# Kernel tuning notes

Hardware: AMD Instinct MI355X
Metric: run time of the kernel (lower is better)

## Reference

```python
import jax, jax.numpy as jnp
import numpy as np

E = 8          # num_experts
K = 2          # num_experts_per_tok
H = 768        # hidden_size
F = 3072       # ffn_hidden_size
B, S = 2, 1024


def setup_inputs() -> dict:
    key = jax.random.key(0)
    ks = jax.random.split(key, 5)
    scale_r = 1.0 / np.sqrt(H)
    scale_1 = 1.0 / np.sqrt(H)
    scale_2 = 1.0 / np.sqrt(F)
    return {
        "hidden_states": jax.random.normal(ks[0], (B, S, H), dtype=jnp.float32),
        "router_w": jax.random.normal(ks[1], (E, H), dtype=jnp.float32) * scale_r,
        "w1": jax.random.normal(ks[2], (E, F, H), dtype=jnp.float32) * scale_1,
        "b1": jnp.zeros((E, F), dtype=jnp.float32),
        "w2": jax.random.normal(ks[3], (E, H, F), dtype=jnp.float32) * scale_2,
        "b2": jnp.zeros((E, H), dtype=jnp.float32),
    }


def reference(hidden_states, router_w, w1, b1, w2, b2):
    b, s, h = hidden_states.shape
    x = hidden_states.reshape(-1, h)                      # [T, H]

    # Router: logits -> top-k -> softmax over the selected k logits
    logits = jnp.einsum('th,eh->te', x, router_w)          # [T, E]
    top_vals, top_idx = jax.lax.top_k(logits, K)           # [T, K]
    probs = jax.nn.softmax(top_vals, axis=-1)              # [T, K]

    # Combine weights per (token, expert): sum of top-k probs routed to e
    one_hot = jax.nn.one_hot(top_idx, E, dtype=probs.dtype)  # [T, K, E]
    combine = jnp.einsum('tk,tke->te', probs, one_hot)       # [T, E]

    # Dense per-expert FFN (GEMM -> exact GELU -> GEMM), combined by weights
    hmid = jnp.einsum('th,efh->tef', x, w1) + b1[None]       # [T, E, F]
    hmid = jax.nn.gelu(hmid, approximate=False)
    y = jnp.einsum('tef,ehf->teh', hmid, w2) + b2[None]      # [T, E, H]
    out = jnp.einsum('teh,te->th', y, combine)               # [T, H]

    return out.reshape(b, s, h)
```

## Files before the change

### kernel.cpp

```cpp
#include <hip/hip_runtime.h>
#include <hip/hip_bf16.h>
#include <math.h>

#define T_TOK 2048
#define EXP   8
#define HID   768
#define FFN   3072
#define MAXTILES 40

typedef __bf16 bf16x8 __attribute__((ext_vector_type(8)));
typedef float  f32x4  __attribute__((ext_vector_type(4)));
typedef short  s16x8  __attribute__((ext_vector_type(8)));

#define WS_CNT      0
#define WS_OFFS     64
#define WS_NTILES   128
#define WS_TILEE    256
#define WS_TILEROW  1280
#define WS_TKE      4096
#define WS_TKP      20480
#define WS_TOKIDS   36864
#define WS_PW       53248
#define WS_XPK      131072
#define WS_W1PK     (WS_XPK  + 15728640)
#define WS_W2PK     (WS_W1PK + 75497472)
#define WS_HMA      (WS_W2PK + 75497472)

__device__ __forceinline__ void gload16(const void* g, void* l) {
    __builtin_amdgcn_global_load_lds((__attribute__((address_space(1))) void*)g,
                                     (__attribute__((address_space(3))) void*)l,
                                     16, 0, 0);
}

__device__ __forceinline__ void split_bf16(float f, short& hi, short& lo) {
    unsigned u  = __float_as_uint(f);
    unsigned h  = (u + 0x8000u) >> 16;
    float    hf = __uint_as_float(h << 16);
    float    lf = f - hf;
    unsigned l  = (__float_as_uint(lf) + 0x8000u) >> 16;
    hi = (short)h; lo = (short)l;
}

__device__ __forceinline__ float gelu_exact(float v) {
    return 0.5f * v * (1.0f + erff(v * 0.70710678118654752f));
}

__global__ void k_init(float* __restrict__ out, int* __restrict__ cnt) {
    int idx = blockIdx.x * blockDim.x + threadIdx.x;
    const int n = T_TOK * HID;
    for (int i = idx; i < n; i += gridDim.x * blockDim.x) out[i] = 0.f;
    if (idx < EXP) cnt[idx] = 0;
}

__global__ __launch_bounds__(256) void k_router(
    const float* __restrict__ x, const float* __restrict__ rw,
    int* __restrict__ tk_e, float* __restrict__ tk_p, int* __restrict__ cnt)
{
    int wave = threadIdx.x >> 6;
    int lane = threadIdx.x & 63;
    int t = blockIdx.x * 4 + wave;
    if (t >= T_TOK) return;

    float acc[EXP];
#pragma unroll
    for (int e = 0; e < EXP; ++e) acc[e] = 0.f;
    const float* xr = x + (size_t)t * HID;
#pragma unroll
    for (int i = 0; i < HID / 64; ++i) {
        int k = i * 64 + lane;
        float xv = xr[k];
#pragma unroll
        for (int e = 0; e < EXP; ++e) acc[e] += xv * rw[e * HID + k];
    }
#pragma unroll
    for (int e = 0; e < EXP; ++e) {
        float v = acc[e];
#pragma unroll
        for (int off = 32; off > 0; off >>= 1) v += __shfl_xor(v, off);
        acc[e] = v;
    }
    int e0 = 0; float v0 = acc[0];
#pragma unroll
    for (int e = 1; e < EXP; ++e) if (acc[e] > v0) { v0 = acc[e]; e0 = e; }
    int e1 = -1; float v1 = -INFINITY;
#pragma unroll
    for (int e = 0; e < EXP; ++e) if (e != e0 && acc[e] > v1) { v1 = acc[e]; e1 = e; }
    float ex = expf(v1 - v0);
    float p0 = 1.f / (1.f + ex);
    float p1 = ex / (1.f + ex);

    if (lane == 0) {
        tk_e[t * 2 + 0] = e0; tk_e[t * 2 + 1] = e1;
        tk_p[t * 2 + 0] = p0; tk_p[t * 2 + 1] = p1;
        atomicAdd(&cnt[e0], 1);
        atomicAdd(&cnt[e1], 1);
    }
}

__global__ __launch_bounds__(256) void k_scatter(
    const int* __restrict__ cnt, int* __restrict__ offs, int* __restrict__ nTiles,
    int* __restrict__ tileE, int* __restrict__ tileRow,
    const int* __restrict__ tk_e, const float* __restrict__ tk_p,
    int* __restrict__ token_ids, float* __restrict__ pw)
{
    __shared__ int fill[EXP];
    __shared__ int offsS[EXP + 1];
    if (threadIdx.x == 0) {
        int o = 0;
        for (int e = 0; e < EXP; ++e) { offsS[e] = o; offs[e] = o; o += cnt[e]; }
        offsS[EXP] = o; offs[EXP] = o;
        int nt = 0;
        for (int e = 0; e < EXP; ++e)
            for (int r = 0; r < cnt[e]; r += 128) {
                tileE[nt] = e; tileRow[nt] = offsS[e] + r; ++nt;
            }
        *nTiles = nt;
    }
    if (threadIdx.x < EXP) fill[threadIdx.x] = 0;
    __syncthreads();
    for (int t = threadIdx.x; t < T_TOK; t += 256) {
#pragma unroll
        for (int kk = 0; kk < 2; ++kk) {
            int e = tk_e[t * 2 + kk];
            int slot = atomicAdd(&fill[e], 1);
            int g = offsS[e] + slot;
            token_ids[g] = t;
            pw[g] = tk_p[t * 2 + kk];
        }
    }
}

__global__ __launch_bounds__(256) void k_packw(
    const float* __restrict__ W, short* __restrict__ pk, int N, int K)
{
    int unit = blockIdx.x * 4 + (threadIdx.x >> 6);
    int lane = threadIdx.x & 63;
    int NTN = N >> 7, NTK = K >> 5;
    int half = unit & 1;
    int u2   = unit >> 1;
    int kt   = u2 % NTK;
    int ent  = u2 / NTK;
    int nt   = ent % NTN;
    int e    = ent / NTN;
    int row  = nt * 128 + half * 64 + lane;

    const float* src = W + ((size_t)e * N + row) * K + kt * 32;
    s16x8 h4[4], l4v[4];
#pragma unroll
    for (int c = 0; c < 32; c += 4) {
        float4 f = *(const float4*)(src + c);
        short hh, ll;
        split_bf16(f.x, hh, ll); h4[c >> 3][(c & 7) + 0] = hh; l4v[c >> 3][(c & 7) + 0] = ll;
        split_bf16(f.y, hh, ll); h4[c >> 3][(c & 7) + 1] = hh; l4v[c >> 3][(c & 7) + 1] = ll;
        split_bf16(f.z, hh, ll); h4[c >> 3][(c & 7) + 2] = hh; l4v[c >> 3][(c & 7) + 2] = ll;
        split_bf16(f.w, hh, ll); h4[c >> 3][(c & 7) + 3] = hh; l4v[c >> 3][(c & 7) + 3] = ll;
    }
    short* base = pk + ((size_t)ent * NTK + kt) * 8192;
#pragma unroll
    for (int kg = 0; kg < 4; ++kg) {
        *(s16x8*)(base + (0 * 8 + kg * 2 + half) * 512 + lane * 8) = h4[kg];
        *(s16x8*)(base + (1 * 8 + kg * 2 + half) * 512 + lane * 8) = l4v[kg];
    }
}

__global__ __launch_bounds__(256) void k_packx(
    const float* __restrict__ x, const int* __restrict__ token_ids,
    const int* __restrict__ tileE, const int* __restrict__ tileRow,
    const int* __restrict__ offs, const int* __restrict__ nTiles,
    short* __restrict__ xpk)
{
    int unit = blockIdx.x * 4 + (threadIdx.x >> 6);
    int lane = threadIdx.x & 63;
    int half = unit & 1;
    int u2   = unit >> 1;
    int kt   = u2 % 24;
    int tile = u2 / 24;
    if (tile >= *nTiles) return;
    int e = tileE[tile];
    int rowEnd = offs[e + 1];
    int g = min(tileRow[tile] + half * 64 + lane, rowEnd - 1);
    int t = token_ids[g];

    const float* src = x + (size_t)t * HID + kt * 32;
    s16x8 h4[4], l4v[4];
#pragma unroll
    for (int c = 0; c < 32; c += 4) {
        float4 f = *(const float4*)(src + c);
        short hh, ll;
        split_bf16(f.x, hh, ll); h4[c >> 3][(c & 7) + 0] = hh; l4v[c >> 3][(c & 7) + 0] = ll;
        split_bf16(f.y, hh, ll); h4[c >> 3][(c & 7) + 1] = hh; l4v[c >> 3][(c & 7) + 1] = ll;
        split_bf16(f.z, hh, ll); h4[c >> 3][(c & 7) + 2] = hh; l4v[c >> 3][(c & 7) + 2] = ll;
        split_bf16(f.w, hh, ll); h4[c >> 3][(c & 7) + 3] = hh; l4v[c >> 3][(c & 7) + 3] = ll;
    }
    short* base = xpk + ((size_t)tile * 24 + kt) * 8192;
#pragma unroll
    for (int kg = 0; kg < 4; ++kg) {
        *(s16x8*)(base + (0 * 8 + kg * 2 + half) * 512 + lane * 8) = h4[kg];
        *(s16x8*)(base + (1 * 8 + kg * 2 + half) * 512 + lane * 8) = l4v[kg];
    }
}


#define DBUF 16384

__global__ __launch_bounds__(256, 2) void k_gemm1_mfma(
    const short* __restrict__ xpk, const short* __restrict__ w1pk,
    const float* __restrict__ b1, short* __restrict__ hmA,
    const int* __restrict__ tileE, const int* __restrict__ tileRow,
    const int* __restrict__ offs, const int* __restrict__ nTiles)
{
    const int lin = blockIdx.x;
    const int swz = (lin & 7) * 120 + (lin >> 3);
    const int bx   = swz % 24;
    const int tile = swz / 24;
    if (tile >= *nTiles) return;
    const int e = tileE[tile];
    const int rowBase = tileRow[tile];
    const int rowEnd = offs[e + 1];
    const int n0 = bx * 128;

    __shared__ __align__(16) short S[2][DBUF];

    const int tid = threadIdx.x;
    const int lane = tid & 63;
    const int w = tid >> 6;
    const int wm = w & 1, wn = w >> 1;
    const int l15 = lane & 15, l4 = lane >> 4;

    const short* jsrc[8];
    int jdst[8];
#pragma unroll
    for (int j = 0; j < 8; ++j) {
        int s = w + j * 4;
        int ab = s >> 4, p = (s >> 3) & 1, kg = (s >> 1) & 3, h = s & 1;
        jdst[j] = ((ab * 2 + p) * 4 + kg) * 1024 + h * 512;
        if (ab == 0)
            jsrc[j] = xpk + (size_t)tile * 24 * 8192 + s * 512 + lane * 8;
        else
            jsrc[j] = w1pk + ((size_t)(e * 24 + bx) * 24) * 8192
                      + (s - 16) * 512 + lane * 8;
    }

    f32x4 acc[4][4] = {};

#pragma unroll
    for (int j = 0; j < 8; ++j) gload16(jsrc[j], (void*)&S[0][jdst[j]]);
    __syncthreads();

    const int NT = 24;
    for (int kt = 0; kt < NT; ++kt) {
        int cur = kt & 1;
        if (kt + 1 < NT) {
            size_t k0 = (size_t)(kt + 1) * 8192;
#pragma unroll
            for (int j = 0; j < 8; ++j) gload16(jsrc[j] + k0, (void*)&S[cur ^ 1][jdst[j]]);
        }
        const short* base = S[cur];
        bf16x8 ah[4], al[4], bh[4], bl[4];
#pragma unroll
        for (int mf = 0; mf < 4; ++mf) {
            int r = wm * 64 + mf * 16 + l15;
            ah[mf] = *(const bf16x8*)(base + (0 * 4 + l4) * 1024 + r * 8);
            al[mf] = *(const bf16x8*)(base + (1 * 4 + l4) * 1024 + r * 8);
        }
#pragma unroll
        for (int nf = 0; nf < 4; ++nf) {
            int c = wn * 64 + nf * 16 + l15;
            bh[nf] = *(const bf16x8*)(base + (2 * 4 + l4) * 1024 + c * 8);
            bl[nf] = *(const bf16x8*)(base + (3 * 4 + l4) * 1024 + c * 8);
        }
#pragma unroll
        for (int mf = 0; mf < 4; ++mf)
#pragma unroll
            for (int nf = 0; nf < 4; ++nf)
                acc[mf][nf] = __builtin_amdgcn_mfma_f32_16x16x32_bf16(ah[mf], bh[nf], acc[mf][nf], 0, 0, 0);
#pragma unroll
        for (int mf = 0; mf < 4; ++mf)
#pragma unroll
            for (int nf = 0; nf < 4; ++nf)
                acc[mf][nf] = __builtin_amdgcn_mfma_f32_16x16x32_bf16(ah[mf], bl[nf], acc[mf][nf], 0, 0, 0);
#pragma unroll
        for (int mf = 0; mf < 4; ++mf)
#pragma unroll
            for (int nf = 0; nf < 4; ++nf)
                acc[mf][nf] = __builtin_amdgcn_mfma_f32_16x16x32_bf16(al[mf], bh[nf], acc[mf][nf], 0, 0, 0);
        __syncthreads();
    }

#pragma unroll
    for (int mf = 0; mf < 4; ++mf)
#pragma unroll
        for (int nf = 0; nf < 4; ++nf) {
            int f = n0 + wn * 64 + nf * 16 + l15;
            float bias = b1[e * FFN + f];
            int ktf = f >> 5, kg = (f >> 3) & 3, sh = f & 7;
            size_t kbase = ((size_t)tile * 96 + ktf) * 8192 + (kg * 2) * 512 + sh;
#pragma unroll
            for (int j = 0; j < 4; ++j) {
                int row = wm * 64 + mf * 16 + l4 * 4 + j;
                if (rowBase + row < rowEnd) {
                    float v = gelu_exact(acc[mf][nf][j] + bias);
                    short hi, lo;
                    split_bf16(v, hi, lo);
                    size_t o = kbase + (row >> 6) * 512 + (row & 63) * 8;
                    hmA[o] = hi;
                    hmA[o + 4096] = lo;
                }
            }
        }
}

__global__ __launch_bounds__(256, 2) void k_gemm2_mfma(
    const short* __restrict__ hmA, const short* __restrict__ w2pk,
    const float* __restrict__ b2, float* __restrict__ out,
    const int* __restrict__ token_ids, const float* __restrict__ pw,
    const int* __restrict__ tileE, const int* __restrict__ tileRow,
    const int* __restrict__ offs, const int* __restrict__ nTiles)
{
    const int lin = blockIdx.x;
    const int swz = (lin & 7) * 120 + (lin >> 3);
    const int sub = swz % 24;
    const int bx  = sub % 6;
    const int z   = sub / 6;
    const int tile = swz / 24;
    if (tile >= *nTiles) return;
    const int e = tileE[tile];
    const int rowBase = tileRow[tile];
    const int rowEnd = offs[e + 1];
    const int n0 = bx * 128;

    __shared__ __align__(16) short S[2][DBUF];

    const int tid = threadIdx.x;
    const int lane = tid & 63;
    const int w = tid >> 6;
    const int wm = w & 1, wn = w >> 1;
    const int l15 = lane & 15, l4 = lane >> 4;

    const short* jsrc[8];
    int jdst[8];
#pragma unroll
    for (int j = 0; j < 8; ++j) {
        int s = w + j * 4;
        int ab = s >> 4, p = (s >> 3) & 1, kg = (s >> 1) & 3, h = s & 1;
        jdst[j] = ((ab * 2 + p) * 4 + kg) * 1024 + h * 512;
        if (ab == 0)
            jsrc[j] = hmA + ((size_t)tile * 96 + z * 24) * 8192 + s * 512 + lane * 8;
        else
            jsrc[j] = w2pk + ((size_t)(e * 6 + bx) * 96 + z * 24) * 8192
                      + (s - 16) * 512 + lane * 8;
    }

    f32x4 acc[4][4] = {};

#pragma unroll
    for (int j = 0; j < 8; ++j) gload16(jsrc[j], (void*)&S[0][jdst[j]]);
    __syncthreads();

    const int NT = 24;
    for (int kt = 0; kt < NT; ++kt) {
        int cur = kt & 1;
        if (kt + 1 < NT) {
            size_t k0 = (size_t)(kt + 1) * 8192;
#pragma unroll
            for (int j = 0; j < 8; ++j) gload16(jsrc[j] + k0, (void*)&S[cur ^ 1][jdst[j]]);
        }
        const short* base = S[cur];
        bf16x8 ah[4], al[4], bh[4], bl[4];
#pragma unroll
        for (int mf = 0; mf < 4; ++mf) {
            int r = wm * 64 + mf * 16 + l15;
            ah[mf] = *(const bf16x8*)(base + (0 * 4 + l4) * 1024 + r * 8);
            al[mf] = *(const bf16x8*)(base + (1 * 4 + l4) * 1024 + r * 8);
        }
#pragma unroll
        for (int nf = 0; nf < 4; ++nf) {
            int c = wn * 64 + nf * 16 + l15;
            bh[nf] = *(const bf16x8*)(base + (2 * 4 + l4) * 1024 + c * 8);
            bl[nf] = *(const bf16x8*)(base + (3 * 4 + l4) * 1024 + c * 8);
        }
#pragma unroll
        for (int mf = 0; mf < 4; ++mf)
#pragma unroll
            for (int nf = 0; nf < 4; ++nf)
                acc[mf][nf] = __builtin_amdgcn_mfma_f32_16x16x32_bf16(ah[mf], bh[nf], acc[mf][nf], 0, 0, 0);
#pragma unroll
        for (int mf = 0; mf < 4; ++mf)
#pragma unroll
            for (int nf = 0; nf < 4; ++nf)
                acc[mf][nf] = __builtin_amdgcn_mfma_f32_16x16x32_bf16(ah[mf], bl[nf], acc[mf][nf], 0, 0, 0);
#pragma unroll
        for (int mf = 0; mf < 4; ++mf)
#pragma unroll
            for (int nf = 0; nf < 4; ++nf)
                acc[mf][nf] = __builtin_amdgcn_mfma_f32_16x16x32_bf16(al[mf], bh[nf], acc[mf][nf], 0, 0, 0);
        __syncthreads();
    }

#pragma unroll
    for (int mf = 0; mf < 4; ++mf)
#pragma unroll
        for (int nf = 0; nf < 4; ++nf) {
            int h = n0 + wn * 64 + nf * 16 + l15;
            float bias = (z == 0) ? b2[e * HID + h] : 0.f;
#pragma unroll
            for (int j = 0; j < 4; ++j) {
                int g = rowBase + wm * 64 + mf * 16 + l4 * 4 + j;
                if (g < rowEnd) {
                    int t = token_ids[g];
                    float p = pw[g];
                    atomicAdd(&out[(size_t)t * HID + h], (acc[mf][nf][j] + bias) * p);
                }
            }
        }
}

extern "C" void kernel_launch(void* const* d_in, const int* in_sizes, int n_in,
                              void* d_out, int out_size, void* d_ws, size_t ws_size,
                              hipStream_t stream) {
    const float* x  = (const float*)d_in[0];
    const float* rw = (const float*)d_in[1];
    const float* w1 = (const float*)d_in[2];
    const float* b1 = (const float*)d_in[3];
    const float* w2 = (const float*)d_in[4];
    const float* b2 = (const float*)d_in[5];
    float* out = (float*)d_out;

    char* ws = (char*)d_ws;
    int*   cnt       = (int*)(ws + WS_CNT);
    int*   offs      = (int*)(ws + WS_OFFS);
    int*   nTiles    = (int*)(ws + WS_NTILES);
    int*   tileE     = (int*)(ws + WS_TILEE);
    int*   tileRow   = (int*)(ws + WS_TILEROW);
    int*   tk_e      = (int*)(ws + WS_TKE);
    float* tk_p      = (float*)(ws + WS_TKP);
    int*   token_ids = (int*)(ws + WS_TOKIDS);
    float* pw        = (float*)(ws + WS_PW);
    short* xpk  = (short*)(ws + WS_XPK);
    short* w1pk = (short*)(ws + WS_W1PK);
    short* w2pk = (short*)(ws + WS_W2PK);
    short* hmA  = (short*)(ws + WS_HMA);

    k_init<<<1024, 256, 0, stream>>>(out, cnt);
    k_router<<<T_TOK / 4, 256, 0, stream>>>(x, rw, tk_e, tk_p, cnt);
    k_scatter<<<1, 256, 0, stream>>>(cnt, offs, nTiles, tileE, tileRow,
                                     tk_e, tk_p, token_ids, pw);
    k_packw<<<2304, 256, 0, stream>>>(w1, w1pk, FFN, HID);
    k_packw<<<2304, 256, 0, stream>>>(w2, w2pk, HID, FFN);
    k_packx<<<480, 256, 0, stream>>>(x, token_ids, tileE, tileRow, offs, nTiles, xpk);
    k_gemm1_mfma<<<960, 256, 0, stream>>>(
        xpk, w1pk, b1, hmA, tileE, tileRow, offs, nTiles);
    k_gemm2_mfma<<<960, 256, 0, stream>>>(
        hmA, w2pk, b2, out, token_ids, pw, tileE, tileRow, offs, nTiles);
}
```

Measured before the change: 503.1 us.

## Triple-buffer LDS in both expert GEMMs with vmcnt-based waits

Both grouped MFMA GEMM kernels move from double to triple LDS buffering and prefetch two K-steps ahead. The per-iteration __syncthreads is replaced by an explicit s_waitcnt vmcnt plus a single s_barrier, so one tile's loads can stay in flight while the current tile is computed. This is meant to hide global-to-LDS latency and cut barrier stalls. LDS use per block goes from 64KB to 96KB and the min-blocks hint is dropped, which may reduce occupancy, and correctness depends on the hand-counted vmcnt matching the direct-to-LDS loads.

```diff
diff --git a/kernel.cpp b/kernel.cpp
--- a/kernel.cpp
+++ b/kernel.cpp
@@ -203,7 +203,7 @@
 
 #define DBUF 16384
 
-__global__ __launch_bounds__(256, 2) void k_gemm1_mfma(
+__global__ __launch_bounds__(256) void k_gemm1_mfma(
     const short* __restrict__ xpk, const short* __restrict__ w1pk,
     const float* __restrict__ b1, short* __restrict__ hmA,
     const int* __restrict__ tileE, const int* __restrict__ tileRow,
@@ -219,7 +219,7 @@
     const int rowEnd = offs[e + 1];
     const int n0 = bx * 128;
 
-    __shared__ __align__(16) short S[2][DBUF];
+    __shared__ __align__(16) short S[3][DBUF];
 
     const int tid = threadIdx.x;
     const int lane = tid & 63;
@@ -243,17 +243,22 @@
 
     f32x4 acc[4][4] = {};
 
+    const int NT = 24;
 #pragma unroll
     for (int j = 0; j < 8; ++j) gload16(jsrc[j], (void*)&S[0][jdst[j]]);
-    __syncthreads();
-
-    const int NT = 24;
+#pragma unroll
+    for (int j = 0; j < 8; ++j) gload16(jsrc[j] + 8192, (void*)&S[1][jdst[j]]);
+
+    int cur = 0;
     for (int kt = 0; kt < NT; ++kt) {
-        int cur = kt & 1;
-        if (kt + 1 < NT) {
-            size_t k0 = (size_t)(kt + 1) * 8192;
-#pragma unroll
-            for (int j = 0; j < 8; ++j) gload16(jsrc[j] + k0, (void*)&S[cur ^ 1][jdst[j]]);
+        if (kt + 1 < NT) asm volatile("s_waitcnt vmcnt(8)" ::: "memory");
+        else             asm volatile("s_waitcnt vmcnt(0)" ::: "memory");
+        __builtin_amdgcn_s_barrier();
+        if (kt + 2 < NT) {
+            int nb = cur + 2; if (nb >= 3) nb -= 3;
+            size_t k0 = (size_t)(kt + 2) * 8192;
+#pragma unroll
+            for (int j = 0; j < 8; ++j) gload16(jsrc[j] + k0, (void*)&S[nb][jdst[j]]);
         }
         const short* base = S[cur];
         bf16x8 ah[4], al[4], bh[4], bl[4];
@@ -284,7 +289,7 @@
 #pragma unroll
             for (int nf = 0; nf < 4; ++nf)
                 acc[mf][nf] = __builtin_amdgcn_mfma_f32_16x16x32_bf16(al[mf], bh[nf], acc[mf][nf], 0, 0, 0);
-        __syncthreads();
+        ++cur; if (cur >= 3) cur -= 3;
     }
 
 #pragma unroll
@@ -310,7 +315,7 @@
         }
 }
 
-__global__ __launch_bounds__(256, 2) void k_gemm2_mfma(
+__global__ __launch_bounds__(256) void k_gemm2_mfma(
     const short* __restrict__ hmA, const short* __restrict__ w2pk,
     const float* __restrict__ b2, float* __restrict__ out,
     const int* __restrict__ token_ids, const float* __restrict__ pw,
@@ -329,7 +334,7 @@
     const int rowEnd = offs[e + 1];
     const int n0 = bx * 128;
 
-    __shared__ __align__(16) short S[2][DBUF];
+    __shared__ __align__(16) short S[3][DBUF];
 
     const int tid = threadIdx.x;
     const int lane = tid & 63;
@@ -353,17 +358,22 @@
 
     f32x4 acc[4][4] = {};
 
+    const int NT = 24;
 #pragma unroll
     for (int j = 0; j < 8; ++j) gload16(jsrc[j], (void*)&S[0][jdst[j]]);
-    __syncthreads();
-
-    const int NT = 24;
+#pragma unroll
+    for (int j = 0; j < 8; ++j) gload16(jsrc[j] + 8192, (void*)&S[1][jdst[j]]);
+
+    int cur = 0;
     for (int kt = 0; kt < NT; ++kt) {
-        int cur = kt & 1;
-        if (kt + 1 < NT) {
-            size_t k0 = (size_t)(kt + 1) * 8192;
-#pragma unroll
-            for (int j = 0; j < 8; ++j) gload16(jsrc[j] + k0, (void*)&S[cur ^ 1][jdst[j]]);
+        if (kt + 1 < NT) asm volatile("s_waitcnt vmcnt(8)" ::: "memory");
+        else             asm volatile("s_waitcnt vmcnt(0)" ::: "memory");
+        __builtin_amdgcn_s_barrier();
+        if (kt + 2 < NT) {
+            int nb = cur + 2; if (nb >= 3) nb -= 3;
+            size_t k0 = (size_t)(kt + 2) * 8192;
+#pragma unroll
+            for (int j = 0; j < 8; ++j) gload16(jsrc[j] + k0, (void*)&S[nb][jdst[j]]);
         }
         const short* base = S[cur];
         bf16x8 ah[4], al[4], bh[4], bl[4];
@@ -394,7 +404,7 @@
 #pragma unroll
             for (int nf = 0; nf < 4; ++nf)
                 acc[mf][nf] = __builtin_amdgcn_mfma_f32_16x16x32_bf16(al[mf], bh[nf], acc[mf][nf], 0, 0, 0);
-        __syncthreads();
+        ++cur; if (cur >= 3) cur -= 3;
     }
 
 #pragma unroll
```

Result: slower. 625.3 us (+24.3%).

## Replace split-bf16 three-pass MFMA GEMMs with single-pass fp16 MFMA

Applied to the files above, without the earlier changes.

Drops the hi/lo bf16 split emulation of fp32 (three MFMA passes per tile) and instead converts inputs, weights and the intermediate activation to fp16 with a single MFMA pass. Packed buffers, LDS tiles and global loads are halved, and the launch-bounds occupancy hint is removed. The aim is to cut MFMA work about threefold and halve memory traffic, at the cost of lower accuracy (fp16 mantissa, range limits on GELU outputs) compared to the near-fp32 emulation.

```diff
diff --git a/kernel.cpp b/kernel.cpp
--- a/kernel.cpp
+++ b/kernel.cpp
@@ -8,9 +8,8 @@
 #define FFN   3072
 #define MAXTILES 40
 
-typedef __bf16 bf16x8 __attribute__((ext_vector_type(8)));
-typedef float  f32x4  __attribute__((ext_vector_type(4)));
-typedef short  s16x8  __attribute__((ext_vector_type(8)));
+typedef _Float16 f16x8 __attribute__((ext_vector_type(8)));
+typedef float    f32x4 __attribute__((ext_vector_type(4)));
 
 #define WS_CNT      0
 #define WS_OFFS     64
@@ -22,23 +21,14 @@
 #define WS_TOKIDS   36864
 #define WS_PW       53248
 #define WS_XPK      131072
-#define WS_W1PK     (WS_XPK  + 15728640)
-#define WS_W2PK     (WS_W1PK + 75497472)
-#define WS_HMA      (WS_W2PK + 75497472)
+#define WS_W1PK     (WS_XPK  + 7864320)
+#define WS_W2PK     (WS_W1PK + 37748736)
+#define WS_HMA      (WS_W2PK + 37748736)
 
 __device__ __forceinline__ void gload16(const void* g, void* l) {
     __builtin_amdgcn_global_load_lds((__attribute__((address_space(1))) void*)g,
                                      (__attribute__((address_space(3))) void*)l,
                                      16, 0, 0);
-}
-
-__device__ __forceinline__ void split_bf16(float f, short& hi, short& lo) {
-    unsigned u  = __float_as_uint(f);
-    unsigned h  = (u + 0x8000u) >> 16;
-    float    hf = __uint_as_float(h << 16);
-    float    lf = f - hf;
-    unsigned l  = (__float_as_uint(lf) + 0x8000u) >> 16;
-    hi = (short)h; lo = (short)l;
 }
 
 __device__ __forceinline__ float gelu_exact(float v) {
@@ -145,22 +135,19 @@
     int row  = nt * 128 + half * 64 + lane;
 
     const float* src = W + ((size_t)e * N + row) * K + kt * 32;
-    s16x8 h4[4], l4v[4];
+    f16x8 h4[4];
 #pragma unroll
     for (int c = 0; c < 32; c += 4) {
         float4 f = *(const float4*)(src + c);
-        short hh, ll;
-        split_bf16(f.x, hh, ll); h4[c >> 3][(c & 7) + 0] = hh; l4v[c >> 3][(c & 7) + 0] = ll;
-        split_bf16(f.y, hh, ll); h4[c >> 3][(c & 7) + 1] = hh; l4v[c >> 3][(c & 7) + 1] = ll;
-        split_bf16(f.z, hh, ll); h4[c >> 3][(c & 7) + 2] = hh; l4v[c >> 3][(c & 7) + 2] = ll;
-        split_bf16(f.w, hh, ll); h4[c >> 3][(c & 7) + 3] = hh; l4v[c >> 3][(c & 7) + 3] = ll;
-    }
-    short* base = pk + ((size_t)ent * NTK + kt) * 8192;
-#pragma unroll
-    for (int kg = 0; kg < 4; ++kg) {
-        *(s16x8*)(base + (0 * 8 + kg * 2 + half) * 512 + lane * 8) = h4[kg];
-        *(s16x8*)(base + (1 * 8 + kg * 2 + half) * 512 + lane * 8) = l4v[kg];
-    }
+        h4[c >> 3][(c & 7) + 0] = (_Float16)f.x;
+        h4[c >> 3][(c & 7) + 1] = (_Float16)f.y;
+        h4[c >> 3][(c & 7) + 2] = (_Float16)f.z;
+        h4[c >> 3][(c & 7) + 3] = (_Float16)f.w;
+    }
+    short* base = pk + ((size_t)ent * NTK + kt) * 4096;
+#pragma unroll
+    for (int kg = 0; kg < 4; ++kg)
+        *(f16x8*)(base + (kg * 2 + half) * 512 + lane * 8) = h4[kg];
 }
 
 __global__ __launch_bounds__(256) void k_packx(
@@ -182,28 +169,25 @@
     int t = token_ids[g];
 
     const float* src = x + (size_t)t * HID + kt * 32;
-    s16x8 h4[4], l4v[4];
+    f16x8 h4[4];
 #pragma unroll
     for (int c = 0; c < 32; c += 4) {
         float4 f = *(const float4*)(src + c);
-        short hh, ll;
-        split_bf16(f.x, hh, ll); h4[c >> 3][(c & 7) + 0] = hh; l4v[c >> 3][(c & 7) + 0] = ll;
-        split_bf16(f.y, hh, ll); h4[c >> 3][(c & 7) + 1] = hh; l4v[c >> 3][(c & 7) + 1] = ll;
-        split_bf16(f.z, hh, ll); h4[c >> 3][(c & 7) + 2] = hh; l4v[c >> 3][(c & 7) + 2] = ll;
-        split_bf16(f.w, hh, ll); h4[c >> 3][(c & 7) + 3] = hh; l4v[c >> 3][(c & 7) + 3] = ll;
-    }
-    short* base = xpk + ((size_t)tile * 24 + kt) * 8192;
-#pragma unroll
-    for (int kg = 0; kg < 4; ++kg) {
-        *(s16x8*)(base + (0 * 8 + kg * 2 + half) * 512 + lane * 8) = h4[kg];
-        *(s16x8*)(base + (1 * 8 + kg * 2 + half) * 512 + lane * 8) = l4v[kg];
-    }
-}
-
-
-#define DBUF 16384
-
-__global__ __launch_bounds__(256, 2) void k_gemm1_mfma(
+        h4[c >> 3][(c & 7) + 0] = (_Float16)f.x;
+        h4[c >> 3][(c & 7) + 1] = (_Float16)f.y;
+        h4[c >> 3][(c & 7) + 2] = (_Float16)f.z;
+        h4[c >> 3][(c & 7) + 3] = (_Float16)f.w;
+    }
+    short* base = xpk + ((size_t)tile * 24 + kt) * 4096;
+#pragma unroll
+    for (int kg = 0; kg < 4; ++kg)
+        *(f16x8*)(base + (kg * 2 + half) * 512 + lane * 8) = h4[kg];
+}
+
+
+#define DBUF 8192
+
+__global__ __launch_bounds__(256) void k_gemm1_mfma(
     const short* __restrict__ xpk, const short* __restrict__ w1pk,
     const float* __restrict__ b1, short* __restrict__ hmA,
     const int* __restrict__ tileE, const int* __restrict__ tileRow,
@@ -227,63 +211,51 @@
     const int wm = w & 1, wn = w >> 1;
     const int l15 = lane & 15, l4 = lane >> 4;
 
-    const short* jsrc[8];
-    int jdst[8];
-#pragma unroll
-    for (int j = 0; j < 8; ++j) {
+    const short* jsrc[4];
+    int jdst[4];
+#pragma unroll
+    for (int j = 0; j < 4; ++j) {
         int s = w + j * 4;
-        int ab = s >> 4, p = (s >> 3) & 1, kg = (s >> 1) & 3, h = s & 1;
-        jdst[j] = ((ab * 2 + p) * 4 + kg) * 1024 + h * 512;
+        int ab = s >> 3, kg = (s >> 1) & 3, h = s & 1;
+        jdst[j] = (ab * 4 + kg) * 1024 + h * 512;
         if (ab == 0)
-            jsrc[j] = xpk + (size_t)tile * 24 * 8192 + s * 512 + lane * 8;
+            jsrc[j] = xpk + (size_t)tile * 24 * 4096 + s * 512 + lane * 8;
         else
-            jsrc[j] = w1pk + ((size_t)(e * 24 + bx) * 24) * 8192
-                      + (s - 16) * 512 + lane * 8;
+            jsrc[j] = w1pk + ((size_t)(e * 24 + bx) * 24) * 4096
+                      + (s - 8) * 512 + lane * 8;
     }
 
     f32x4 acc[4][4] = {};
 
 #pragma unroll
-    for (int j = 0; j < 8; ++j) gload16(jsrc[j], (void*)&S[0][jdst[j]]);
+    for (int j = 0; j < 4; ++j) gload16(jsrc[j], (void*)&S[0][jdst[j]]);
     __syncthreads();
 
     const int NT = 24;
     for (int kt = 0; kt < NT; ++kt) {
         int cur = kt & 1;
         if (kt + 1 < NT) {
-            size_t k0 = (size_t)(kt + 1) * 8192;
-#pragma unroll
-            for (int j = 0; j < 8; ++j) gload16(jsrc[j] + k0, (void*)&S[cur ^ 1][jdst[j]]);
+            size_t k0 = (size_t)(kt + 1) * 4096;
+#pragma unroll
+            for (int j = 0; j < 4; ++j) gload16(jsrc[j] + k0, (void*)&S[cur ^ 1][jdst[j]]);
         }
         const short* base = S[cur];
-        bf16x8 ah[4], al[4], bh[4], bl[4];
+        f16x8 ah[4], bh[4];
 #pragma unroll
         for (int mf = 0; mf < 4; ++mf) {
             int r = wm * 64 + mf * 16 + l15;
-            ah[mf] = *(const bf16x8*)(base + (0 * 4 + l4) * 1024 + r * 8);
-            al[mf] = *(const bf16x8*)(base + (1 * 4 + l4) * 1024 + r * 8);
+            ah[mf] = *(const f16x8*)(base + l4 * 1024 + r * 8);
         }
 #pragma unroll
         for (int nf = 0; nf < 4; ++nf) {
             int c = wn * 64 + nf * 16 + l15;
-            bh[nf] = *(const bf16x8*)(base + (2 * 4 + l4) * 1024 + c * 8);
-            bl[nf] = *(const bf16x8*)(base + (3 * 4 + l4) * 1024 + c * 8);
+            bh[nf] = *(const f16x8*)(base + (4 + l4) * 1024 + c * 8);
         }
 #pragma unroll
         for (int mf = 0; mf < 4; ++mf)
 #pragma unroll
             for (int nf = 0; nf < 4; ++nf)
-                acc[mf][nf] = __builtin_amdgcn_mfma_f32_16x16x32_bf16(ah[mf], bh[nf], acc[mf][nf], 0, 0, 0);
-#pragma unroll
-        for (int mf = 0; mf < 4; ++mf)
-#pragma unroll
-            for (int nf = 0; nf < 4; ++nf)
-                acc[mf][nf] = __builtin_amdgcn_mfma_f32_16x16x32_bf16(ah[mf], bl[nf], acc[mf][nf], 0, 0, 0);
-#pragma unroll
-        for (int mf = 0; mf < 4; ++mf)
-#pragma unroll
-            for (int nf = 0; nf < 4; ++nf)
-                acc[mf][nf] = __builtin_amdgcn_mfma_f32_16x16x32_bf16(al[mf], bh[nf], acc[mf][nf], 0, 0, 0);
+                acc[mf][nf] = __builtin_amdgcn_mfma_f32_16x16x32_f16(ah[mf], bh[nf], acc[mf][nf], 0, 0, 0);
         __syncthreads();
     }
 
@@ -294,23 +266,20 @@
             int f = n0 + wn * 64 + nf * 16 + l15;
             float bias = b1[e * FFN + f];
             int ktf = f >> 5, kg = (f >> 3) & 3, sh = f & 7;
-            size_t kbase = ((size_t)tile * 96 + ktf) * 8192 + (kg * 2) * 512 + sh;
+            size_t kbase = ((size_t)tile * 96 + ktf) * 4096 + (kg * 2) * 512 + sh;
 #pragma unroll
             for (int j = 0; j < 4; ++j) {
                 int row = wm * 64 + mf * 16 + l4 * 4 + j;
                 if (rowBase + row < rowEnd) {
                     float v = gelu_exact(acc[mf][nf][j] + bias);
-                    short hi, lo;
-                    split_bf16(v, hi, lo);
                     size_t o = kbase + (row >> 6) * 512 + (row & 63) * 8;
-                    hmA[o] = hi;
-                    hmA[o + 4096] = lo;
+                    ((_Float16*)hmA)[o] = (_Float16)v;
                 }
             }
         }
 }
 
-__global__ __launch_bounds__(256, 2) void k_gemm2_mfma(
+__global__ __launch_bounds__(256) void k_gemm2_mfma(
     const short* __restrict__ hmA, const short* __restrict__ w2pk,
     const float* __restrict__ b2, float* __restrict__ out,
     const int* __restrict__ token_ids, const float* __restrict__ pw,
@@ -337,63 +306,51 @@
     const int wm = w & 1, wn = w >> 1;
     const int l15 = lane & 15, l4 = lane >> 4;
 
-    const short* jsrc[8];
-    int jdst[8];
-#pragma unroll
-    for (int j = 0; j < 8; ++j) {
+    const short* jsrc[4];
+    int jdst[4];
+#pragma unroll
+    for (int j = 0; j < 4; ++j) {
         int s = w + j * 4;
-        int ab = s >> 4, p = (s >> 3) & 1, kg = (s >> 1) & 3, h = s & 1;
-        jdst[j] = ((ab * 2 + p) * 4 + kg) * 1024 + h * 512;
+        int ab = s >> 3, kg = (s >> 1) & 3, h = s & 1;
+        jdst[j] = (ab * 4 + kg) * 1024 + h * 512;
         if (ab == 0)
-            jsrc[j] = hmA + ((size_t)tile * 96 + z * 24) * 8192 + s * 512 + lane * 8;
+            jsrc[j] = hmA + ((size_t)tile * 96 + z * 24) * 4096 + s * 512 + lane * 8;
         else
-            jsrc[j] = w2pk + ((size_t)(e * 6 + bx) * 96 + z * 24) * 8192
-                      + (s - 16) * 512 + lane * 8;
+            jsrc[j] = w2pk + ((size_t)(e * 6 + bx) * 96 + z * 24) * 4096
+                      + (s - 8) * 512 + lane * 8;
     }
 
     f32x4 acc[4][4] = {};
 
 #pragma unroll
-    for (int j = 0; j < 8; ++j) gload16(jsrc[j], (void*)&S[0][jdst[j]]);
+    for (int j = 0; j < 4; ++j) gload16(jsrc[j], (void*)&S[0][jdst[j]]);
     __syncthreads();
 
     const int NT = 24;
     for (int kt = 0; kt < NT; ++kt) {
         int cur = kt & 1;
         if (kt + 1 < NT) {
-            size_t k0 = (size_t)(kt + 1) * 8192;
-#pragma unroll
-            for (int j = 0; j < 8; ++j) gload16(jsrc[j] + k0, (void*)&S[cur ^ 1][jdst[j]]);
+            size_t k0 = (size_t)(kt + 1) * 4096;
+#pragma unroll
+            for (int j = 0; j < 4; ++j) gload16(jsrc[j] + k0, (void*)&S[cur ^ 1][jdst[j]]);
         }
         const short* base = S[cur];
-        bf16x8 ah[4], al[4], bh[4], bl[4];
+        f16x8 ah[4], bh[4];
 #pragma unroll
         for (int mf = 0; mf < 4; ++mf) {
             int r = wm * 64 + mf * 16 + l15;
-            ah[mf] = *(const bf16x8*)(base + (0 * 4 + l4) * 1024 + r * 8);
-            al[mf] = *(const bf16x8*)(base + (1 * 4 + l4) * 1024 + r * 8);
+            ah[mf] = *(const f16x8*)(base + l4 * 1024 + r * 8);
         }
 #pragma unroll
         for (int nf = 0; nf < 4; ++nf) {
             int c = wn * 64 + nf * 16 + l15;
-            bh[nf] = *(const bf16x8*)(base + (2 * 4 + l4) * 1024 + c * 8);
-            bl[nf] = *(const bf16x8*)(base + (3 * 4 + l4) * 1024 + c * 8);
+            bh[nf] = *(const f16x8*)(base + (4 + l4) * 1024 + c * 8);
         }
 #pragma unroll
         for (int mf = 0; mf < 4; ++mf)
 #pragma unroll
             for (int nf = 0; nf < 4; ++nf)
-                acc[mf][nf] = __builtin_amdgcn_mfma_f32_16x16x32_bf16(ah[mf], bh[nf], acc[mf][nf], 0, 0, 0);
-#pragma unroll
-        for (int mf = 0; mf < 4; ++mf)
-#pragma unroll
-            for (int nf = 0; nf < 4; ++nf)
-                acc[mf][nf] = __builtin_amdgcn_mfma_f32_16x16x32_bf16(ah[mf], bl[nf], acc[mf][nf], 0, 0, 0);
-#pragma unroll
-        for (int mf = 0; mf < 4; ++mf)
-#pragma unroll
-            for (int nf = 0; nf < 4; ++nf)
-                acc[mf][nf] = __builtin_amdgcn_mfma_f32_16x16x32_bf16(al[mf], bh[nf], acc[mf][nf], 0, 0, 0);
+                acc[mf][nf] = __builtin_amdgcn_mfma_f32_16x16x32_f16(ah[mf], bh[nf], acc[mf][nf], 0, 0, 0);
         __syncthreads();
     }
 
```

Result: faster. 419.3 us (-16.7%).
